# Kernel tuning notes

Measured on AMD Instinct MI355X. Metric: run time of the kernel, lower is better.

Reference implementation:

```python
import jax, jax.numpy as jnp
import numpy as np

B, H, S, D = 2, 16, 2048, 128


def setup_inputs() -> dict:
    key = jax.random.key(0)
    kq, kk, kv = jax.random.split(key, 3)
    q = jax.random.normal(kq, (B, H, S, D), dtype=jnp.float32)
    k = jax.random.normal(kk, (B, H, S, D), dtype=jnp.float32)
    v = jax.random.normal(kv, (B, H, S, D), dtype=jnp.float32)
    scale = jnp.float32(1.0 / np.sqrt(D))
    return {"q": q, "k": k, "v": v, "scale": scale}


def reference(q, k, v, scale):
    # scores: [B, H, S, S]
    attn = jnp.einsum("bhqd,bhkd->bhqk", q, k) * scale
    attn = jnp.square(jax.nn.relu(attn))  # relu(x)^2 score function (no softmax)
    return jnp.einsum("bhqk,bhkd->bhqd", attn, v)
```

## Files before the change

### kernel.cpp

```cpp
#include <hip/hip_runtime.h>
#include <hip/hip_bf16.h>
#include <stdint.h>

#define S_LEN 2048
#define D_DIM 128
#define QT 128
#define KT 64
#define NT (S_LEN/KT)

typedef float  f32x4  __attribute__((ext_vector_type(4)));
typedef short  bf16x8 __attribute__((ext_vector_type(8)));
typedef short  bf16x4 __attribute__((ext_vector_type(4)));

__device__ __forceinline__ short f2bf(float f) {
    return __builtin_bit_cast(short, __float2bfloat16(f));
}

__device__ __forceinline__ void gload_lds16(const short* g, short* l) {
    __builtin_amdgcn_global_load_lds(
        (const __attribute__((address_space(1))) void*)g,
        (__attribute__((address_space(3))) void*)l,
        16, 0, 0);
}

__global__ __launch_bounds__(256)
void convert_k_kernel(const float* __restrict__ kin, short* __restrict__ kbf) {
    const size_t i = ((size_t)blockIdx.x * 256 + threadIdx.x) * 8;
    f32x4 a = *(const f32x4*)(kin + i);
    f32x4 c = *(const f32x4*)(kin + i + 4);
    bf16x8 t;
    t[0]=f2bf(a[0]); t[1]=f2bf(a[1]); t[2]=f2bf(a[2]); t[3]=f2bf(a[3]);
    t[4]=f2bf(c[0]); t[5]=f2bf(c[1]); t[6]=f2bf(c[2]); t[7]=f2bf(c[3]);
    *(bf16x8*)(kbf + i) = t;
}

__global__ __launch_bounds__(256)
void transpose_v_kernel(const float* __restrict__ vin, short* __restrict__ vt) {
    __shared__ short T[16 * 130];
    const int tid = threadIdx.x;
    const int blk = blockIdx.x;
    const int bh  = blk >> 3;
    const int d0  = (blk & 7) * 16;
    const float* vb = vin + (size_t)bh * S_LEN * D_DIM;
    short* vtb = vt + (size_t)bh * (size_t)D_DIM * S_LEN;
    const int c4 = tid & 3;
    const int rr = tid >> 2;
    const int dl = tid >> 4;
    const int kc = tid & 15;

    for (int kc0 = 0; kc0 < S_LEN; kc0 += 128) {
        #pragma unroll
        for (int h = 0; h < 2; ++h) {
            const int krow = kc0 + h*64 + rr;
            f32x4 a = *(const f32x4*)(vb + (size_t)krow * D_DIM + d0 + c4*4);
            #pragma unroll
            for (int j = 0; j < 4; ++j)
                T[(c4*4 + j)*130 + h*64 + rr] = f2bf(a[j]);
        }
        __syncthreads();
        int w0 = *(const int*)&T[dl*130 + kc*8 + 0];
        int w1 = *(const int*)&T[dl*130 + kc*8 + 2];
        int w2 = *(const int*)&T[dl*130 + kc*8 + 4];
        int w3 = *(const int*)&T[dl*130 + kc*8 + 6];
        int4 val = make_int4(w0, w1, w2, w3);
        *(int4*)(vtb + (size_t)(d0 + dl) * S_LEN + kc0 + kc*8) = val;
        __syncthreads();
    }
}

#define KOFF(B) ((B)*8192)
#define VOFF(B) (16384 + (B)*8192)
#define POFF 32768

__global__ __launch_bounds__(256, 2)
void relu2_attn_main(const float* __restrict__ q,
                     const short* __restrict__ kbf,
                     const short* __restrict__ vtbf,
                     const float* __restrict__ scale_p,
                     float* __restrict__ out) {
    __shared__ short lds[40960];

    const int tid  = threadIdx.x;
    const int wave = tid >> 6;
    const int lane = tid & 63;
    const int l15  = lane & 15;
    const int lg   = lane >> 4;
    const int swz  = l15 & 7;

    const int bid = blockIdx.x;
    const int bh  = bid & 31;
    const int qt  = bid >> 5;
    const int q0  = qt * QT;

    const float* qb = q    + (size_t)bh * S_LEN * D_DIM;
    const short* kb = kbf  + (size_t)bh * S_LEN * D_DIM;
    const short* vt = vtbf + (size_t)bh * (size_t)D_DIM * S_LEN;
    float*       ob = out  + (size_t)bh * S_LEN * D_DIM;

    const float scale = scale_p[0];

    bf16x8 qa[2][4];
    {
        const int qrow = q0 + wave * 32;
        #pragma unroll
        for (int qf = 0; qf < 2; ++qf) {
            const float* qp = qb + (size_t)(qrow + qf*16 + l15) * D_DIM + lg * 8;
            #pragma unroll
            for (int dk = 0; dk < 4; ++dk) {
                f32x4 a = *(const f32x4*)(qp + dk*32);
                f32x4 c = *(const f32x4*)(qp + dk*32 + 4);
                bf16x8 t;
                t[0]=f2bf(a[0]*scale); t[1]=f2bf(a[1]*scale);
                t[2]=f2bf(a[2]*scale); t[3]=f2bf(a[3]*scale);
                t[4]=f2bf(c[0]*scale); t[5]=f2bf(c[1]*scale);
                t[6]=f2bf(c[2]*scale); t[7]=f2bf(c[3]*scale);
                qa[qf][dk] = t;
            }
        }
    }

    f32x4 oacc[2][8];
    #pragma unroll
    for (int i = 0; i < 2; ++i)
        #pragma unroll
        for (int j = 0; j < 8; ++j)
            oacc[i][j] = f32x4{0.f, 0.f, 0.f, 0.f};

#define STAGE(T, B) do {                                                      \
    const int k0_ = (T) * KT;                                                 \
    _Pragma("unroll")                                                         \
    for (int p_ = 0; p_ < 4; ++p_) {                                          \
        const int ch_ = p_*4 + wave;                                          \
        const int r_  = ch_*4 + (lane >> 4);                 \
        gload_lds16(kb + (((size_t)(k0_ + r_)) << 7)                          \
                       + (((lane & 15) ^ (r_ & 7)) << 3),                     \
                    &lds[KOFF(B) + ch_*512]);                                 \
        const int d_  = ch_*8 + (lane >> 3);            \
        gload_lds16(vt + (((size_t)d_) << 11) + k0_                           \
                       + (((lane & 7) ^ (d_ & 7)) << 3),                      \
                    &lds[VOFF(B) + ch_*512]);                                 \
    }                                                                         \
} while (0)

    STAGE(0, 0);

    for (int t = 0; t < NT; ++t) {
        const int b = t & 1;
        __syncthreads();
        if (t + 1 < NT) STAGE(t + 1, b ^ 1);

        f32x4 sacc[2][4];
        #pragma unroll
        for (int qf = 0; qf < 2; ++qf)
            #pragma unroll
            for (int kf = 0; kf < 4; ++kf)
                sacc[qf][kf] = f32x4{0.f, 0.f, 0.f, 0.f};

        #pragma unroll
        for (int dk = 0; dk < 4; ++dk) {
            #pragma unroll
            for (int kf = 0; kf < 4; ++kf) {
                const int krow = kf*16 + l15;
                bf16x8 af = *(const bf16x8*)
                    &lds[KOFF(b) + krow*128 + (((dk*4 + lg) ^ swz) << 3)];
                #pragma unroll
                for (int qf = 0; qf < 2; ++qf)
                    sacc[qf][kf] = __builtin_amdgcn_mfma_f32_16x16x32_bf16(
                        af, qa[qf][dk], sacc[qf][kf], 0, 0, 0);
            }
        }

        #pragma unroll
        for (int qf = 0; qf < 2; ++qf) {
            const int qrow = wave*32 + qf*16 + l15;
            #pragma unroll
            for (int kf = 0; kf < 4; ++kf) {
                f32x4 sv = sacc[qf][kf];
                bf16x4 w;
                #pragma unroll
                for (int e = 0; e < 4; ++e) {
                    float r0 = fmaxf(sv[e], 0.f);
                    w[e] = f2bf(r0 * r0);
                }
                *(bf16x4*)&lds[POFF + qrow*64 + ((kf*16 + lg*4) ^ (swz << 3))] = w;
            }
        }

        #pragma unroll
        for (int ks = 0; ks < 2; ++ks) {
            bf16x8 pa[2];
            #pragma unroll
            for (int qf = 0; qf < 2; ++qf) {
                const int qrow = wave*32 + qf*16 + l15;
                pa[qf] = *(const bf16x8*)
                    &lds[POFF + qrow*64 + ((ks*32 + lg*8) ^ (swz << 3))];
            }
            #pragma unroll
            for (int df = 0; df < 8; ++df) {
                const int drow = df*16 + l15;
                bf16x8 vf = *(const bf16x8*)
                    &lds[VOFF(b) + drow*64 + (((ks*4 + lg) ^ swz) << 3)];
                #pragma unroll
                for (int qf = 0; qf < 2; ++qf)
                    oacc[qf][df] = __builtin_amdgcn_mfma_f32_16x16x32_bf16(
                        pa[qf], vf, oacc[qf][df], 0, 0, 0);
            }
        }
    }

    #pragma unroll
    for (int qf = 0; qf < 2; ++qf) {
        #pragma unroll
        for (int df = 0; df < 8; ++df) {
            f32x4 o = oacc[qf][df];
            const int row = q0 + wave*32 + qf*16 + lg*4;
            float* op = ob + (size_t)row * D_DIM + df*16 + l15;
            op[0*D_DIM] = o[0];
            op[1*D_DIM] = o[1];
            op[2*D_DIM] = o[2];
            op[3*D_DIM] = o[3];
        }
    }
}

#define KS 136
#define VS 72
#define PS 72

__global__ __launch_bounds__(256, 2)
void relu2_attn_fallback(const float* __restrict__ q,
                         const float* __restrict__ k,
                         const float* __restrict__ v,
                         const float* __restrict__ scale_p,
                         float* __restrict__ out) {
    __shared__ short Klds[KT][KS];
    __shared__ short VTlds[D_DIM][VS];
    __shared__ short Plds[QT][PS];

    const int tid  = threadIdx.x;
    const int wave = tid >> 6;
    const int lane = tid & 63;
    const int l15  = lane & 15;
    const int lg   = lane >> 4;

    const int bid = blockIdx.x;
    const int bh  = bid & 31;
    const int qt  = bid >> 5;
    const int q0  = qt * QT;

    const float* qb = q + (size_t)bh * S_LEN * D_DIM;
    const float* kb = k + (size_t)bh * S_LEN * D_DIM;
    const float* vb = v + (size_t)bh * S_LEN * D_DIM;
    float*       ob = out + (size_t)bh * S_LEN * D_DIM;

    const float scale = scale_p[0];

    bf16x8 qa[2][4];
    {
        const int qrow = q0 + wave * 32;
        #pragma unroll
        for (int qf = 0; qf < 2; ++qf) {
            const float* qp = qb + (size_t)(qrow + qf*16 + l15) * D_DIM + lg * 8;
            #pragma unroll
            for (int dk = 0; dk < 4; ++dk) {
                f32x4 a = *(const f32x4*)(qp + dk*32);
                f32x4 c = *(const f32x4*)(qp + dk*32 + 4);
                bf16x8 t;
                t[0]=f2bf(a[0]*scale); t[1]=f2bf(a[1]*scale);
                t[2]=f2bf(a[2]*scale); t[3]=f2bf(a[3]*scale);
                t[4]=f2bf(c[0]*scale); t[5]=f2bf(c[1]*scale);
                t[6]=f2bf(c[2]*scale); t[7]=f2bf(c[3]*scale);
                qa[qf][dk] = t;
            }
        }
    }

    const int kr = tid >> 4;
    const int kc = tid & 15;
    const int vd = tid & 127;
    const int vh = (tid >> 7) * 32;

    f32x4 kreg[8];
    float vreg[32];

#define FLOAD_TILE(T) do {                                                    \
    const float* kp_ = kb + (size_t)((T) * KT) * D_DIM;                       \
    _Pragma("unroll")                                                         \
    for (int p = 0; p < 4; ++p) {                                             \
        const float* rp_ = kp_ + (size_t)(p*16 + kr) * D_DIM + kc*8;          \
        kreg[2*p]   = *(const f32x4*)rp_;                                     \
        kreg[2*p+1] = *(const f32x4*)(rp_ + 4);                               \
    }                                                                         \
    const float* vp_ = vb + (size_t)((T) * KT + vh) * D_DIM + vd;             \
    _Pragma("unroll")                                                         \
    for (int j = 0; j < 32; ++j) vreg[j] = vp_[(size_t)j * D_DIM];            \
} while (0)

#define FSTORE_TILE() do {                                                    \
    _Pragma("unroll")                                                         \
    for (int p = 0; p < 4; ++p) {                                             \
        f32x4 a_ = kreg[2*p], b_ = kreg[2*p+1];                               \
        bf16x8 w_;                                                            \
        w_[0]=f2bf(a_[0]); w_[1]=f2bf(a_[1]); w_[2]=f2bf(a_[2]); w_[3]=f2bf(a_[3]); \
        w_[4]=f2bf(b_[0]); w_[5]=f2bf(b_[1]); w_[6]=f2bf(b_[2]); w_[7]=f2bf(b_[3]); \
        *(bf16x8*)&Klds[p*16 + kr][kc*8] = w_;                                \
    }                                                                         \
    _Pragma("unroll")                                                         \
    for (int c = 0; c < 4; ++c) {                                             \
        bf16x8 w_;                                                            \
        w_[0]=f2bf(vreg[c*8+0]); w_[1]=f2bf(vreg[c*8+1]);                     \
        w_[2]=f2bf(vreg[c*8+2]); w_[3]=f2bf(vreg[c*8+3]);                     \
        w_[4]=f2bf(vreg[c*8+4]); w_[5]=f2bf(vreg[c*8+5]);                     \
        w_[6]=f2bf(vreg[c*8+6]); w_[7]=f2bf(vreg[c*8+7]);                     \
        *(bf16x8*)&VTlds[vd][vh + c*8] = w_;                                  \
    }                                                                         \
} while (0)

    f32x4 oacc[2][8];
    #pragma unroll
    for (int i = 0; i < 2; ++i)
        #pragma unroll
        for (int j = 0; j < 8; ++j)
            oacc[i][j] = f32x4{0.f, 0.f, 0.f, 0.f};

    FLOAD_TILE(0);

    for (int t = 0; t < NT; ++t) {
        FSTORE_TILE();
        __syncthreads();
        FLOAD_TILE((t + 1) & (NT - 1));

        f32x4 sacc[2][4];
        #pragma unroll
        for (int qf = 0; qf < 2; ++qf)
            #pragma unroll
            for (int kf = 0; kf < 4; ++kf)
                sacc[qf][kf] = f32x4{0.f, 0.f, 0.f, 0.f};

        #pragma unroll
        for (int dk = 0; dk < 4; ++dk) {
            #pragma unroll
            for (int kf = 0; kf < 4; ++kf) {
                bf16x8 bf = *(const bf16x8*)&Klds[kf*16 + l15][dk*32 + lg*8];
                #pragma unroll
                for (int qf = 0; qf < 2; ++qf)
                    sacc[qf][kf] = __builtin_amdgcn_mfma_f32_16x16x32_bf16(
                        qa[qf][dk], bf, sacc[qf][kf], 0, 0, 0);
            }
        }

        #pragma unroll
        for (int qf = 0; qf < 2; ++qf) {
            #pragma unroll
            for (int kf = 0; kf < 4; ++kf) {
                f32x4 sv = sacc[qf][kf];
                #pragma unroll
                for (int e = 0; e < 4; ++e) {
                    float r = fmaxf(sv[e], 0.f);
                    Plds[wave*32 + qf*16 + lg*4 + e][kf*16 + l15] = f2bf(r * r);
                }
            }
        }

        #pragma unroll
        for (int ks = 0; ks < 2; ++ks) {
            bf16x8 pa[2];
            #pragma unroll
            for (int qf = 0; qf < 2; ++qf)
                pa[qf] = *(const bf16x8*)&Plds[wave*32 + qf*16 + l15][ks*32 + lg*8];
            #pragma unroll
            for (int df = 0; df < 8; ++df) {
                bf16x8 vf = *(const bf16x8*)&VTlds[df*16 + l15][ks*32 + lg*8];
                #pragma unroll
                for (int qf = 0; qf < 2; ++qf)
                    oacc[qf][df] = __builtin_amdgcn_mfma_f32_16x16x32_bf16(
                        pa[qf], vf, oacc[qf][df], 0, 0, 0);
            }
        }
        __syncthreads();
    }

    #pragma unroll
    for (int qf = 0; qf < 2; ++qf) {
        #pragma unroll
        for (int df = 0; df < 8; ++df) {
            f32x4 o = oacc[qf][df];
            const int row = q0 + wave*32 + qf*16 + lg*4;
            float* op = ob + (size_t)row * D_DIM + df*16 + l15;
            op[0*D_DIM] = o[0];
            op[1*D_DIM] = o[1];
            op[2*D_DIM] = o[2];
            op[3*D_DIM] = o[3];
        }
    }
}

extern "C" void kernel_launch(void* const* d_in, const int* in_sizes, int n_in,
                              void* d_out, int out_size, void* d_ws, size_t ws_size,
                              hipStream_t stream) {
    const float* q = (const float*)d_in[0];
    const float* k = (const float*)d_in[1];
    const float* v = (const float*)d_in[2];
    const float* scale = (const float*)d_in[3];
    float* out = (float*)d_out;

    const size_t elems = (size_t)2 * 16 * S_LEN * D_DIM;
    const size_t need  = elems * 2 * 2;

    if (ws_size >= need) {
        short* kbf = (short*)d_ws;
        short* vtb = (short*)d_ws + elems;
        convert_k_kernel<<<dim3((int)(elems / (256 * 8))), dim3(256), 0, stream>>>(k, kbf);
        transpose_v_kernel<<<dim3(256), dim3(256), 0, stream>>>(v, vtb);
        relu2_attn_main<<<dim3(512), dim3(256), 0, stream>>>(q, kbf, vtb, scale, out);
    } else {
        relu2_attn_fallback<<<dim3(512), dim3(256), 0, stream>>>(q, k, v, scale, out);
    }
}
```

Before: 97.94 us.

## Switch main attention kernel to 32x32x16 MFMA with register-resident P

Rewrites the main relu² attention loop to use 32x32x16 bf16 MFMAs. The relu² scores are converted to the PV operand layout in registers with packed bf16 converts and permlane32 swaps, so the P round trip through LDS and its barrier go away. The KV loop is unrolled by two with fixed buffer indices, the LDS buffers grow to 64 KB, and s_setprio hints are placed around the MFMA sections. The aim is fewer LDS accesses and instructions per tile, but the larger LDS footprint and the f32x16 accumulators may limit occupancy to two blocks per CU.

```diff
diff --git a/kernel.cpp b/kernel.cpp
--- a/kernel.cpp
+++ b/kernel.cpp
@@ -9,11 +9,19 @@
 #define NT (S_LEN/KT)
 
 typedef float  f32x4  __attribute__((ext_vector_type(4)));
+typedef float  f32x16 __attribute__((ext_vector_type(16)));
 typedef short  bf16x8 __attribute__((ext_vector_type(8)));
 typedef short  bf16x4 __attribute__((ext_vector_type(4)));
+typedef unsigned int uintx4 __attribute__((ext_vector_type(4)));
 
 __device__ __forceinline__ short f2bf(float f) {
     return __builtin_bit_cast(short, __float2bfloat16(f));
+}
+
+__device__ __forceinline__ unsigned int pk2(float lo, float hi) {
+    unsigned int d;
+    asm("v_cvt_pk_bf16_f32 %0, %1, %2" : "=v"(d) : "v"(lo), "v"(hi));
+    return d;
 }
 
 __device__ __forceinline__ void gload_lds16(const short* g, short* l) {
@@ -68,34 +76,171 @@
     }
 }
 
-#define KOFF(B) ((B)*8192)
-#define VOFF(B) (16384 + (B)*8192)
-#define POFF 32768
-
 __global__ __launch_bounds__(256, 2)
 void relu2_attn_main(const float* __restrict__ q,
                      const short* __restrict__ kbf,
                      const short* __restrict__ vtbf,
                      const float* __restrict__ scale_p,
                      float* __restrict__ out) {
-    __shared__ short lds[40960];
+    __shared__ __align__(16) char lds[65536];
+
+    const int tid  = threadIdx.x;
+    const int wave = tid >> 6;
+    const int lane = tid & 63;
+    const int l31  = lane & 31;
+    const int hi   = lane >> 5;
+    const int swz  = l31 & 7;
+
+    const int bid = blockIdx.x;
+    const int bh  = bid & 31;
+    const int qt  = bid >> 5;
+    const int q0  = qt * QT;
+
+    const float* qb = q    + (size_t)bh * S_LEN * D_DIM;
+    const short* kb = kbf  + (size_t)bh * S_LEN * D_DIM;
+    const short* vt = vtbf + (size_t)bh * (size_t)D_DIM * S_LEN;
+    float*       ob = out  + (size_t)bh * S_LEN * D_DIM;
+
+    const float scale = scale_p[0];
+
+    const int KB = l31*256 + ((hi ^ swz) << 4);
+    const int VB = 32768 + l31*128 + ((hi ^ swz) << 4);
+
+    bf16x8 qa[8];
+    {
+        const int qrow = q0 + wave*32 + l31;
+        const float* qp = qb + (size_t)qrow * D_DIM + hi*8;
+        #pragma unroll
+        for (int dk = 0; dk < 8; ++dk) {
+            f32x4 a = *(const f32x4*)(qp + dk*16);
+            f32x4 c = *(const f32x4*)(qp + dk*16 + 4);
+            bf16x8 t;
+            t[0]=f2bf(a[0]*scale); t[1]=f2bf(a[1]*scale);
+            t[2]=f2bf(a[2]*scale); t[3]=f2bf(a[3]*scale);
+            t[4]=f2bf(c[0]*scale); t[5]=f2bf(c[1]*scale);
+            t[6]=f2bf(c[2]*scale); t[7]=f2bf(c[3]*scale);
+            qa[dk] = t;
+        }
+    }
+
+    f32x16 oacc[4];
+    #pragma unroll
+    for (int df = 0; df < 4; ++df) oacc[df] = {};
+
+#define STAGE(T, B) do {                                                      \
+    const int k0_ = (T) * KT;                                                 \
+    _Pragma("unroll")                                                         \
+    for (int p_ = 0; p_ < 4; ++p_) {                                          \
+        const int ch_ = p_*4 + wave;                                          \
+        const int r_  = ch_*4 + (lane >> 4);                 \
+        gload_lds16(kb + (((size_t)(k0_ + r_)) << 7)                          \
+                       + (((lane & 15) ^ (r_ & 7)) << 3),                     \
+                    (short*)(lds + (B)*16384 + ch_*1024));                    \
+        const int d_  = ch_*8 + (lane >> 3);           \
+        gload_lds16(vt + (((size_t)d_) << 11) + k0_                           \
+                       + (((lane & 7) ^ (d_ & 7)) << 3),                      \
+                    (short*)(lds + 32768 + (B)*16384 + ch_*1024));            \
+    }                                                                         \
+} while (0)
+
+#define TILE_COMPUTE(BUF) do {                                                \
+    f32x16 s0 = {}, s1 = {};                                                  \
+    __builtin_amdgcn_s_setprio(1);                                            \
+    _Pragma("unroll")                                                         \
+    for (int dk = 0; dk < 8; ++dk) {                                          \
+        bf16x8 a0 = *(const bf16x8*)(lds + ((KB ^ (dk<<5)) | ((BUF)<<14)));   \
+        bf16x8 a1 = *(const bf16x8*)(lds + ((KB ^ (dk<<5)) | (1<<13) | ((BUF)<<14))); \
+        s0 = __builtin_amdgcn_mfma_f32_32x32x16_bf16(a0, qa[dk], s0, 0, 0, 0);\
+        s1 = __builtin_amdgcn_mfma_f32_32x32x16_bf16(a1, qa[dk], s1, 0, 0, 0);\
+    }                                                                         \
+    __builtin_amdgcn_s_setprio(0);                                            \
+              \
+    bf16x8 pa[4];                                                             \
+    _Pragma("unroll")                                                         \
+    for (int kf = 0; kf < 2; ++kf) {                                          \
+        const f32x16 sv = kf ? s1 : s0;                                       \
+        float pr[16];                                                         \
+        _Pragma("unroll")                                                     \
+        for (int r = 0; r < 16; ++r) {                                        \
+            float m_ = fmaxf(sv[r], 0.f); pr[r] = m_ * m_;                    \
+        }                                                                     \
+        _Pragma("unroll")                                                     \
+        for (int t2 = 0; t2 < 2; ++t2) {                                      \
+            unsigned int X  = pk2(pr[8*t2+0], pr[8*t2+1]);                    \
+            unsigned int Y  = pk2(pr[8*t2+4], pr[8*t2+5]);                    \
+            unsigned int X2 = pk2(pr[8*t2+2], pr[8*t2+3]);                    \
+            unsigned int Y2 = pk2(pr[8*t2+6], pr[8*t2+7]);                    \
+            asm volatile("v_permlane32_swap_b32 %0, %1" : "+v"(X),  "+v"(Y)); \
+            asm volatile("v_permlane32_swap_b32 %0, %1" : "+v"(X2), "+v"(Y2));\
+            pa[kf*2 + t2] = __builtin_bit_cast(bf16x8, (uintx4){X, X2, Y, Y2});\
+        }                                                                     \
+    }                                                                         \
+    __builtin_amdgcn_s_setprio(1);                                            \
+    _Pragma("unroll")                                                         \
+    for (int s_ = 0; s_ < 4; ++s_) {                                          \
+        _Pragma("unroll")                                                     \
+        for (int df = 0; df < 4; ++df) {                                      \
+            bf16x8 vf = *(const bf16x8*)(lds + ((VB ^ (s_<<5)) | (df<<12) | ((BUF)<<14))); \
+            oacc[df] = __builtin_amdgcn_mfma_f32_32x32x16_bf16(pa[s_], vf, oacc[df], 0, 0, 0); \
+        }                                                                     \
+    }                                                                         \
+    __builtin_amdgcn_s_setprio(0);                                            \
+} while (0)
+
+    STAGE(0, 0);
+
+    #pragma unroll 1
+    for (int p = 0; p < NT/2; ++p) {
+        __syncthreads();
+        STAGE(2*p + 1, 1);
+        TILE_COMPUTE(0);
+        __syncthreads();
+        STAGE((2*p + 2) & (NT - 1), 0);
+        TILE_COMPUTE(1);
+    }
+
+    #pragma unroll
+    for (int df = 0; df < 4; ++df) {
+        #pragma unroll
+        for (int rg = 0; rg < 4; ++rg) {
+            #pragma unroll
+            for (int e = 0; e < 4; ++e) {
+                const int row = q0 + wave*32 + rg*8 + hi*4 + e;
+                ob[(size_t)row * D_DIM + df*32 + l31] = oacc[df][rg*4 + e];
+            }
+        }
+    }
+}
+
+#define KS 136
+#define VS 72
+#define PS 72
+
+__global__ __launch_bounds__(256, 2)
+void relu2_attn_fallback(const float* __restrict__ q,
+                         const float* __restrict__ k,
+                         const float* __restrict__ v,
+                         const float* __restrict__ scale_p,
+                         float* __restrict__ out) {
+    __shared__ short Klds[KT][KS];
+    __shared__ short VTlds[D_DIM][VS];
+    __shared__ short Plds[QT][PS];
 
     const int tid  = threadIdx.x;
     const int wave = tid >> 6;
     const int lane = tid & 63;
     const int l15  = lane & 15;
     const int lg   = lane >> 4;
-    const int swz  = l15 & 7;
 
     const int bid = blockIdx.x;
     const int bh  = bid & 31;
     const int qt  = bid >> 5;
     const int q0  = qt * QT;
 
-    const float* qb = q    + (size_t)bh * S_LEN * D_DIM;
-    const short* kb = kbf  + (size_t)bh * S_LEN * D_DIM;
-    const short* vt = vtbf + (size_t)bh * (size_t)D_DIM * S_LEN;
-    float*       ob = out  + (size_t)bh * S_LEN * D_DIM;
+    const float* qb = q + (size_t)bh * S_LEN * D_DIM;
+    const float* kb = k + (size_t)bh * S_LEN * D_DIM;
+    const float* vb = v + (size_t)bh * S_LEN * D_DIM;
+    float*       ob = out + (size_t)bh * S_LEN * D_DIM;
 
     const float scale = scale_p[0];
 
@@ -119,6 +264,47 @@
         }
     }
 
+    const int kr = tid >> 4;
+    const int kc = tid & 15;
+    const int vd = tid & 127;
+    const int vh = (tid >> 7) * 32;
+
+    f32x4 kreg[8];
+    float vreg[32];
+
+#define FLOAD_TILE(T) do {                                                    \
+    const float* kp_ = kb + (size_t)((T) * KT) * D_DIM;                       \
+    _Pragma("unroll")                                                         \
+    for (int p = 0; p < 4; ++p) {                                             \
+        const float* rp_ = kp_ + (size_t)(p*16 + kr) * D_DIM + kc*8;          \
+        kreg[2*p]   = *(const f32x4*)rp_;                                     \
+        kreg[2*p+1] = *(const f32x4*)(rp_ + 4);                               \
+    }                                                                         \
+    const float* vp_ = vb + (size_t)((T) * KT + vh) * D_DIM + vd;             \
+    _Pragma("unroll")                                                         \
+    for (int j = 0; j < 32; ++j) vreg[j] = vp_[(size_t)j * D_DIM];            \
+} while (0)
+
+#define FSTORE_TILE() do {                                                    \
+    _Pragma("unroll")                                                         \
+    for (int p = 0; p < 4; ++p) {                                             \
+        f32x4 a_ = kreg[2*p], b_ = kreg[2*p+1];                               \
+        bf16x8 w_;                                                            \
+        w_[0]=f2bf(a_[0]); w_[1]=f2bf(a_[1]); w_[2]=f2bf(a_[2]); w_[3]=f2bf(a_[3]); \
+        w_[4]=f2bf(b_[0]); w_[5]=f2bf(b_[1]); w_[6]=f2bf(b_[2]); w_[7]=f2bf(b_[3]); \
+        *(bf16x8*)&Klds[p*16 + kr][kc*8] = w_;                                \
+    }                                                                         \
+    _Pragma("unroll")                                                         \
+    for (int c = 0; c < 4; ++c) {                                             \
+        bf16x8 w_;                                                            \
+        w_[0]=f2bf(vreg[c*8+0]); w_[1]=f2bf(vreg[c*8+1]);                     \
+        w_[2]=f2bf(vreg[c*8+2]); w_[3]=f2bf(vreg[c*8+3]);                     \
+        w_[4]=f2bf(vreg[c*8+4]); w_[5]=f2bf(vreg[c*8+5]);                     \
+        w_[6]=f2bf(vreg[c*8+6]); w_[7]=f2bf(vreg[c*8+7]);                     \
+        *(bf16x8*)&VTlds[vd][vh + c*8] = w_;                                  \
+    }                                                                         \
+} while (0)
+
     f32x4 oacc[2][8];
     #pragma unroll
     for (int i = 0; i < 2; ++i)
@@ -126,28 +312,12 @@
         for (int j = 0; j < 8; ++j)
             oacc[i][j] = f32x4{0.f, 0.f, 0.f, 0.f};
 
-#define STAGE(T, B) do {                                                      \
-    const int k0_ = (T) * KT;                                                 \
-    _Pragma("unroll")                                                         \
-    for (int p_ = 0; p_ < 4; ++p_) {                                          \
-        const int ch_ = p_*4 + wave;                                          \
-        const int r_  = ch_*4 + (lane >> 4);                 \
-        gload_lds16(kb + (((size_t)(k0_ + r_)) << 7)                          \
-                       + (((lane & 15) ^ (r_ & 7)) << 3),                     \
-                    &lds[KOFF(B) + ch_*512]);                                 \
-        const int d_  = ch_*8 + (lane >> 3);            \
-        gload_lds16(vt + (((size_t)d_) << 11) + k0_                           \
-                       + (((lane & 7) ^ (d_ & 7)) << 3),                      \
-                    &lds[VOFF(B) + ch_*512]);                                 \
-    }                                                                         \
-} while (0)
-
-    STAGE(0, 0);
+    FLOAD_TILE(0);
 
     for (int t = 0; t < NT; ++t) {
-        const int b = t & 1;
-        __syncthreads();
-        if (t + 1 < NT) STAGE(t + 1, b ^ 1);
+        FSTORE_TILE();
+        __syncthreads();
+        FLOAD_TILE((t + 1) & (NT - 1));
 
         f32x4 sacc[2][4];
         #pragma unroll
@@ -160,29 +330,24 @@
         for (int dk = 0; dk < 4; ++dk) {
             #pragma unroll
             for (int kf = 0; kf < 4; ++kf) {
-                const int krow = kf*16 + l15;
-                bf16x8 af = *(const bf16x8*)
-                    &lds[KOFF(b) + krow*128 + (((dk*4 + lg) ^ swz) << 3)];
+                bf16x8 bf = *(const bf16x8*)&Klds[kf*16 + l15][dk*32 + lg*8];
                 #pragma unroll
                 for (int qf = 0; qf < 2; ++qf)
                     sacc[qf][kf] = __builtin_amdgcn_mfma_f32_16x16x32_bf16(
-                        af, qa[qf][dk], sacc[qf][kf], 0, 0, 0);
+                        qa[qf][dk], bf, sacc[qf][kf], 0, 0, 0);
             }
         }
 
         #pragma unroll
         for (int qf = 0; qf < 2; ++qf) {
-            const int qrow = wave*32 + qf*16 + l15;
             #pragma unroll
             for (int kf = 0; kf < 4; ++kf) {
                 f32x4 sv = sacc[qf][kf];
-                bf16x4 w;
                 #pragma unroll
                 for (int e = 0; e < 4; ++e) {
-                    float r0 = fmaxf(sv[e], 0.f);
-                    w[e] = f2bf(r0 * r0);
+                    float r = fmaxf(sv[e], 0.f);
+                    Plds[wave*32 + qf*16 + lg*4 + e][kf*16 + l15] = f2bf(r * r);
                 }
-                *(bf16x4*)&lds[POFF + qrow*64 + ((kf*16 + lg*4) ^ (swz << 3))] = w;
             }
         }
 
@@ -190,22 +355,18 @@
         for (int ks = 0; ks < 2; ++ks) {
             bf16x8 pa[2];
             #pragma unroll
-            for (int qf = 0; qf < 2; ++qf) {
-                const int qrow = wave*32 + qf*16 + l15;
-                pa[qf] = *(const bf16x8*)
-                    &lds[POFF + qrow*64 + ((ks*32 + lg*8) ^ (swz << 3))];
-            }
+            for (int qf = 0; qf < 2; ++qf)
+                pa[qf] = *(const bf16x8*)&Plds[wave*32 + qf*16 + l15][ks*32 + lg*8];
             #pragma unroll
             for (int df = 0; df < 8; ++df) {
-                const int drow = df*16 + l15;
-                bf16x8 vf = *(const bf16x8*)
-                    &lds[VOFF(b) + drow*64 + (((ks*4 + lg) ^ swz) << 3)];
+                bf16x8 vf = *(const bf16x8*)&VTlds[df*16 + l15][ks*32 + lg*8];
                 #pragma unroll
                 for (int qf = 0; qf < 2; ++qf)
                     oacc[qf][df] = __builtin_amdgcn_mfma_f32_16x16x32_bf16(
                         pa[qf], vf, oacc[qf][df], 0, 0, 0);
             }
         }
+        __syncthreads();
     }
 
     #pragma unroll
@@ -223,178 +384,6 @@
     }
 }
 
-#define KS 136
-#define VS 72
-#define PS 72
-
-__global__ __launch_bounds__(256, 2)
-void relu2_attn_fallback(const float* __restrict__ q,
-                         const float* __restrict__ k,
-                         const float* __restrict__ v,
-                         const float* __restrict__ scale_p,
-                         float* __restrict__ out) {
-    __shared__ short Klds[KT][KS];
-    __shared__ short VTlds[D_DIM][VS];
-    __shared__ short Plds[QT][PS];
-
-    const int tid  = threadIdx.x;
-    const int wave = tid >> 6;
-    const int lane = tid & 63;
-    const int l15  = lane & 15;
-    const int lg   = lane >> 4;
-
-    const int bid = blockIdx.x;
-    const int bh  = bid & 31;
-    const int qt  = bid >> 5;
-    const int q0  = qt * QT;
-
-    const float* qb = q + (size_t)bh * S_LEN * D_DIM;
-    const float* kb = k + (size_t)bh * S_LEN * D_DIM;
-    const float* vb = v + (size_t)bh * S_LEN * D_DIM;
-    float*       ob = out + (size_t)bh * S_LEN * D_DIM;
-
-    const float scale = scale_p[0];
-
-    bf16x8 qa[2][4];
-    {
-        const int qrow = q0 + wave * 32;
-        #pragma unroll
-        for (int qf = 0; qf < 2; ++qf) {
-            const float* qp = qb + (size_t)(qrow + qf*16 + l15) * D_DIM + lg * 8;
-            #pragma unroll
-            for (int dk = 0; dk < 4; ++dk) {
-                f32x4 a = *(const f32x4*)(qp + dk*32);
-                f32x4 c = *(const f32x4*)(qp + dk*32 + 4);
-                bf16x8 t;
-                t[0]=f2bf(a[0]*scale); t[1]=f2bf(a[1]*scale);
-                t[2]=f2bf(a[2]*scale); t[3]=f2bf(a[3]*scale);
-                t[4]=f2bf(c[0]*scale); t[5]=f2bf(c[1]*scale);
-                t[6]=f2bf(c[2]*scale); t[7]=f2bf(c[3]*scale);
-                qa[qf][dk] = t;
-            }
-        }
-    }
-
-    const int kr = tid >> 4;
-    const int kc = tid & 15;
-    const int vd = tid & 127;
-    const int vh = (tid >> 7) * 32;
-
-    f32x4 kreg[8];
-    float vreg[32];
-
-#define FLOAD_TILE(T) do {                                                    \
-    const float* kp_ = kb + (size_t)((T) * KT) * D_DIM;                       \
-    _Pragma("unroll")                                                         \
-    for (int p = 0; p < 4; ++p) {                                             \
-        const float* rp_ = kp_ + (size_t)(p*16 + kr) * D_DIM + kc*8;          \
-        kreg[2*p]   = *(const f32x4*)rp_;                                     \
-        kreg[2*p+1] = *(const f32x4*)(rp_ + 4);                               \
-    }                                                                         \
-    const float* vp_ = vb + (size_t)((T) * KT + vh) * D_DIM + vd;             \
-    _Pragma("unroll")                                                         \
-    for (int j = 0; j < 32; ++j) vreg[j] = vp_[(size_t)j * D_DIM];            \
-} while (0)
-
-#define FSTORE_TILE() do {                                                    \
-    _Pragma("unroll")                                                         \
-    for (int p = 0; p < 4; ++p) {                                             \
-        f32x4 a_ = kreg[2*p], b_ = kreg[2*p+1];                               \
-        bf16x8 w_;                                                            \
-        w_[0]=f2bf(a_[0]); w_[1]=f2bf(a_[1]); w_[2]=f2bf(a_[2]); w_[3]=f2bf(a_[3]); \
-        w_[4]=f2bf(b_[0]); w_[5]=f2bf(b_[1]); w_[6]=f2bf(b_[2]); w_[7]=f2bf(b_[3]); \
-        *(bf16x8*)&Klds[p*16 + kr][kc*8] = w_;                                \
-    }                                                                         \
-    _Pragma("unroll")                                                         \
-    for (int c = 0; c < 4; ++c) {                                             \
-        bf16x8 w_;                                                            \
-        w_[0]=f2bf(vreg[c*8+0]); w_[1]=f2bf(vreg[c*8+1]);                     \
-        w_[2]=f2bf(vreg[c*8+2]); w_[3]=f2bf(vreg[c*8+3]);                     \
-        w_[4]=f2bf(vreg[c*8+4]); w_[5]=f2bf(vreg[c*8+5]);                     \
-        w_[6]=f2bf(vreg[c*8+6]); w_[7]=f2bf(vreg[c*8+7]);                     \
-        *(bf16x8*)&VTlds[vd][vh + c*8] = w_;                                  \
-    }                                                                         \
-} while (0)
-
-    f32x4 oacc[2][8];
-    #pragma unroll
-    for (int i = 0; i < 2; ++i)
-        #pragma unroll
-        for (int j = 0; j < 8; ++j)
-            oacc[i][j] = f32x4{0.f, 0.f, 0.f, 0.f};
-
-    FLOAD_TILE(0);
-
-    for (int t = 0; t < NT; ++t) {
-        FSTORE_TILE();
-        __syncthreads();
-        FLOAD_TILE((t + 1) & (NT - 1));
-
-        f32x4 sacc[2][4];
-        #pragma unroll
-        for (int qf = 0; qf < 2; ++qf)
-            #pragma unroll
-            for (int kf = 0; kf < 4; ++kf)
-                sacc[qf][kf] = f32x4{0.f, 0.f, 0.f, 0.f};
-
-        #pragma unroll
-        for (int dk = 0; dk < 4; ++dk) {
-            #pragma unroll
-            for (int kf = 0; kf < 4; ++kf) {
-                bf16x8 bf = *(const bf16x8*)&Klds[kf*16 + l15][dk*32 + lg*8];
-                #pragma unroll
-                for (int qf = 0; qf < 2; ++qf)
-                    sacc[qf][kf] = __builtin_amdgcn_mfma_f32_16x16x32_bf16(
-                        qa[qf][dk], bf, sacc[qf][kf], 0, 0, 0);
-            }
-        }
-
-        #pragma unroll
-        for (int qf = 0; qf < 2; ++qf) {
-            #pragma unroll
-            for (int kf = 0; kf < 4; ++kf) {
-                f32x4 sv = sacc[qf][kf];
-                #pragma unroll
-                for (int e = 0; e < 4; ++e) {
-                    float r = fmaxf(sv[e], 0.f);
-                    Plds[wave*32 + qf*16 + lg*4 + e][kf*16 + l15] = f2bf(r * r);
-                }
-            }
-        }
-
-        #pragma unroll
-        for (int ks = 0; ks < 2; ++ks) {
-            bf16x8 pa[2];
-            #pragma unroll
-            for (int qf = 0; qf < 2; ++qf)
-                pa[qf] = *(const bf16x8*)&Plds[wave*32 + qf*16 + l15][ks*32 + lg*8];
-            #pragma unroll
-            for (int df = 0; df < 8; ++df) {
-                bf16x8 vf = *(const bf16x8*)&VTlds[df*16 + l15][ks*32 + lg*8];
-                #pragma unroll
-                for (int qf = 0; qf < 2; ++qf)
-                    oacc[qf][df] = __builtin_amdgcn_mfma_f32_16x16x32_bf16(
-                        pa[qf], vf, oacc[qf][df], 0, 0, 0);
-            }
-        }
-        __syncthreads();
-    }
-
-    #pragma unroll
-    for (int qf = 0; qf < 2; ++qf) {
-        #pragma unroll
-        for (int df = 0; df < 8; ++df) {
-            f32x4 o = oacc[qf][df];
-            const int row = q0 + wave*32 + qf*16 + lg*4;
-            float* op = ob + (size_t)row * D_DIM + df*16 + l15;
-            op[0*D_DIM] = o[0];
-            op[1*D_DIM] = o[1];
-            op[2*D_DIM] = o[2];
-            op[3*D_DIM] = o[3];
-        }
-    }
-}
-
 extern "C" void kernel_launch(void* const* d_in, const int* in_sizes, int n_in,
                               void* d_out, int out_size, void* d_ws, size_t ws_size,
                               hipStream_t stream) {
```

Measured after the change: 97.80 us. No clear change (-0.1%).
